# Kernel tuning notes

Measured on AMD Instinct MI355X. Metric: run time of the kernel, lower is better.

The kernel has to match this reference:

```python
import jax, jax.numpy as jnp
import numpy as np

# Mamba2 config fixed by MambaIndexer.__init__: d_state=64, expand=1, headdim=32
D_MODEL = 1024
D_STATE = 64
EXPAND = 1
D_INNER = EXPAND * D_MODEL          # 1024
HEADDIM = 32
NHEADS = D_INNER // HEADDIM         # 32
D_CONV = 4
NGROUPS = 1
IDX_DIM = 64
SEQ = 2048
CONV_DIM = D_INNER + 2 * NGROUPS * D_STATE            # 1152 (x, B, C share the conv)
D_IN_PROJ = 2 * D_INNER + 2 * NGROUPS * D_STATE + NHEADS  # 2208 (z, xBC, dt)


def setup_inputs() -> dict:
    key = jax.random.key(0)
    ks = jax.random.split(key, 10)
    s = 0.02  # init scale for projection weights
    return {
        "x": jax.random.normal(ks[0], (SEQ, D_MODEL), jnp.float32),
        "W_in": jax.random.normal(ks[1], (D_MODEL, D_IN_PROJ), jnp.float32) * s,
        "conv_w": jax.random.normal(ks[2], (CONV_DIM, D_CONV), jnp.float32) * s,
        "conv_b": jnp.zeros((CONV_DIM,), jnp.float32),
        "dt_bias": jax.random.normal(ks[3], (NHEADS,), jnp.float32) * 0.1,
        "A_log": jax.random.uniform(ks[4], (NHEADS,), jnp.float32, 0.0, 1.5),
        "D": jax.random.normal(ks[5], (NHEADS,), jnp.float32),
        "norm_w": jnp.ones((D_INNER,), jnp.float32),
        "W_out": jax.random.normal(ks[6], (D_INNER, D_MODEL), jnp.float32) * s,
        "Wq": jax.random.normal(ks[7], (D_MODEL, IDX_DIM), jnp.float32) * s,
        "Wk": jax.random.normal(ks[8], (D_MODEL, IDX_DIM), jnp.float32) * s,
    }


def _mamba2(x, W_in, conv_w, conv_b, dt_bias, A_log, D, norm_w, W_out):
    L = x.shape[0]
    zxbcdt = x @ W_in                                   # (L, 2208)
    z = zxbcdt[:, :D_INNER]                             # gate
    xBC = zxbcdt[:, D_INNER:D_INNER + CONV_DIM]
    dt = jax.nn.softplus(zxbcdt[:, D_INNER + CONV_DIM:] + dt_bias)  # (L, H)
    # causal depthwise conv1d over seq, kernel 4, then silu
    conv = jax.lax.conv_general_dilated(
        xBC.T[None],                                    # (1, C, L)
        conv_w[:, None, :],                             # (C, 1, K)
        (1,), [(D_CONV - 1, 0)], feature_group_count=CONV_DIM)
    xBC = jax.nn.silu(conv[0].T + conv_b)               # (L, C)
    xs = xBC[:, :D_INNER].reshape(L, NHEADS, HEADDIM)   # (L, H, P)
    B = xBC[:, D_INNER:D_INNER + D_STATE]               # (L, N), ngroups=1
    C = xBC[:, D_INNER + D_STATE:]                      # (L, N)
    A = -jnp.exp(A_log)                                 # (H,)
    dA = jnp.exp(dt * A)                                # (L, H)
    dBx = jnp.einsum('lh,lhp,ln->lhpn', dt, xs, B)      # (L, H, P, N)

    def step(h, inp):
        dA_t, dBx_t, C_t = inp
        h = dA_t[:, None, None] * h + dBx_t             # (H, P, N)
        return h, jnp.einsum('hpn,n->hp', h, C_t)

    h0 = jnp.zeros((NHEADS, HEADDIM, D_STATE), x.dtype)
    _, y = jax.lax.scan(step, h0, (dA, dBx, C))         # y: (L, H, P)
    y = y + D[:, None] * xs                             # skip connection
    y = y.reshape(L, D_INNER) * jax.nn.silu(z)          # gated
    y = y * jax.lax.rsqrt(jnp.mean(y * y, axis=-1, keepdims=True) + 1e-5) * norm_w
    return y @ W_out                                    # (L, d_model)


def reference(x, W_in, conv_w, conv_b, dt_bias, A_log, D, norm_w, W_out, Wq, Wk):
    L = x.shape[0]
    x_mamba = _mamba2(x, W_in, conv_w, conv_b, dt_bias, A_log, D, norm_w, W_out)
    q = x_mamba @ Wq                                    # (L, idx)
    k = x @ Wk                                          # (L, idx)
    scores = jnp.einsum('ti,si->ts', q, k) * (IDX_DIM ** -0.5)
    mask = jnp.tril(jnp.ones((L, L), dtype=bool))
    return jnp.where(mask, scores, -jnp.inf)
```

## Files before the change

kernel.cpp:

```cpp
#include <hip/hip_runtime.h>
#include <hip/hip_bf16.h>
#include <math.h>
#include <float.h>

#define SEQ 2048
#define DMODEL 1024
#define DINNER 1024
#define DSTATE 64
#define HEADDIM 32
#define NHEADS 32
#define DCONV 4
#define CONVDIM 1152
#define DINPROJ 2208
#define DINPROJ_PAD 2304
#define IDXDIM 64

#define CHUNK 64
#define NCHUNKS (SEQ / CHUNK)

#define MASK_VAL (-1e30f)

typedef unsigned short u16;
typedef __bf16 bf16x8 __attribute__((ext_vector_type(8)));
typedef float f32x4 __attribute__((ext_vector_type(4)));
typedef u16 u16x8 __attribute__((ext_vector_type(8)));

__device__ __forceinline__ u16 f2bf(float x) {
    unsigned int u = __float_as_uint(x);
    u += 0x7FFFu + ((u >> 16) & 1u);
    return (u16)(u >> 16);
}
__device__ __forceinline__ float bf2f(u16 u) {
    return __uint_as_float(((unsigned int)u) << 16);
}
__device__ __forceinline__ bf16x8 asbf(u16x8 v) {
    union { u16x8 u; bf16x8 b; } c; c.u = v; return c.b;
}

__device__ __forceinline__ void gload_lds16(const void* g, void* l) {
    __builtin_amdgcn_global_load_lds(
        (const __attribute__((address_space(1))) void*)g,
        (__attribute__((address_space(3))) void*)l, 16, 0, 0);
}

__global__ __launch_bounds__(256)
void convert_all(const float* __restrict__ x, u16* __restrict__ xb,
                 const float* __restrict__ W_in, u16* __restrict__ Wt_in,
                 const float* __restrict__ Wk, u16* __restrict__ Wt_k) {
    __shared__ float tile[32][33];
    int b = blockIdx.x, tid = threadIdx.x;

    if (b < 2048) {
        int i = (b * 256 + tid) * 4;
        float4 v = *(const float4*)(x + i);
        ushort4 o;
        o.x = f2bf(v.x); o.y = f2bf(v.y); o.z = f2bf(v.z); o.w = f2bf(v.w);
        *(ushort4*)(xb + i) = o;
        return;
    }
    const float* W; u16* Wt; int N, bx, by;
    if (b < 4352) { int l = b - 2048; W = W_in; Wt = Wt_in; N = DINPROJ; bx = l % 72; by = l / 72; }
    else          { int l = b - 4352; W = Wk;   Wt = Wt_k;  N = IDXDIM;  bx = l & 1;  by = l >> 1; }
    int k0 = by * 32, n0 = bx * 32;
    int tj = tid & 31, ti = tid >> 5;
#pragma unroll
    for (int s = 0; s < 4; s++) {
        int i = ti + s * 8;
        float v = 0.f;
        if (n0 + tj < N) v = W[(size_t)(k0 + i) * N + n0 + tj];
        tile[i][tj] = v;
    }
    __syncthreads();
#pragma unroll
    for (int s = 0; s < 4; s++) {
        int i = ti + s * 8;
        Wt[(size_t)(n0 + i) * DMODEL + k0 + tj] = f2bf(tile[tj][i]);
    }
}

template<int BM, int BN, int WM, int WN, bool OUT_BF16>
__device__ __forceinline__
void gemm_body(u16* As, u16* Bs,
               const u16* __restrict__ A, const u16* __restrict__ Bt,
               void* __restrict__ Cout, int N, int K, int bx, int by) {
    constexpr int BK = 64;
    constexpr int SLOTS = BK / 8;
    constexpr int MI = WM / 16, NI = WN / 16;
    constexpr int WCOLS = BN / WN;
    constexpr int A_ISS = (BM * BK * 2) / (256 * 16);
    constexpr int B_ISS = (BN * BK * 2) / (256 * 16);

    const int tid = threadIdx.x;
    const int lane = tid & 63;
    const int wid = tid >> 6;
    const int wbase = wid * 64;
    const int wr = wid / WCOLS, wc = wid % WCOLS;
    const int row0 = by * BM, col0 = bx * BN;

    f32x4 acc[MI][NI];
#pragma unroll
    for (int m = 0; m < MI; m++)
#pragma unroll
        for (int n = 0; n < NI; n++) acc[m][n] = (f32x4){0.f, 0.f, 0.f, 0.f};

    const int lrow = lane & 15, lkg = lane >> 4;

    for (int kb = 0; kb < K; kb += BK) {
#pragma unroll
        for (int i = 0; i < A_ISS; i++) {
            int e = (i * 256 + tid) * 8;
            int r = e / BK;
            int sl = (e >> 3) & (SLOTS - 1);
            int c = ((sl ^ (r & (SLOTS - 1))) << 3);
            gload_lds16(A + (size_t)(row0 + r) * K + kb + c,
                        &As[(i * 256 + wbase) * 8]);
        }
#pragma unroll
        for (int i = 0; i < B_ISS; i++) {
            int e = (i * 256 + tid) * 8;
            int r = e / BK;
            int sl = (e >> 3) & (SLOTS - 1);
            int c = ((sl ^ (r & (SLOTS - 1))) << 3);
            gload_lds16(Bt + (size_t)(col0 + r) * K + kb + c,
                        &Bs[(i * 256 + wbase) * 8]);
        }
        __syncthreads();

#pragma unroll
        for (int ks = 0; ks < BK / 32; ks++) {
            bf16x8 af[MI], bff[NI];
#pragma unroll
            for (int m = 0; m < MI; m++) {
                int row = wr * WM + m * 16 + lrow;
                int koff = ks * 32 + lkg * 8;
                af[m] = *(const bf16x8*)&As[row * BK + (koff ^ ((row & (SLOTS - 1)) << 3))];
            }
#pragma unroll
            for (int n = 0; n < NI; n++) {
                int row = wc * WN + n * 16 + lrow;
                int koff = ks * 32 + lkg * 8;
                bff[n] = *(const bf16x8*)&Bs[row * BK + (koff ^ ((row & (SLOTS - 1)) << 3))];
            }
#pragma unroll
            for (int m = 0; m < MI; m++)
#pragma unroll
                for (int n = 0; n < NI; n++)
                    acc[m][n] = __builtin_amdgcn_mfma_f32_16x16x32_bf16(
                        af[m], bff[n], acc[m][n], 0, 0, 0);
        }
        __syncthreads();
    }

    const int crow = (lane >> 4) * 4;
    const int ccol = lane & 15;
#pragma unroll
    for (int m = 0; m < MI; m++) {
#pragma unroll
        for (int n = 0; n < NI; n++) {
            int col = col0 + wc * WN + n * 16 + ccol;
            if (col < N) {
                size_t base = (size_t)(row0 + wr * WM + m * 16 + crow) * N + col;
#pragma unroll
                for (int r = 0; r < 4; r++) {
                    if (OUT_BF16)
                        ((u16*)Cout)[base + (size_t)r * N] = f2bf(acc[m][n][r]);
                    else
                        ((float*)Cout)[base + (size_t)r * N] = acc[m][n][r];
                }
            }
        }
    }
}

__global__ __launch_bounds__(256)
void gemm1_k(const u16* __restrict__ xb, const u16* __restrict__ Wt_in,
             u16* __restrict__ zx_bf, const u16* __restrict__ Wt_k,
             u16* __restrict__ kb,
             const float* __restrict__ Wq, const float* __restrict__ W_out,
             const float* __restrict__ norm_w, u16* __restrict__ Wt_nq) {
    extern __shared__ __align__(16) u16 sm[];
    int b = blockIdx.x, tid = threadIdx.x;
    if (b < 288) {
        gemm_body<128, 128, 64, 64, true>(sm, sm + 128 * 64, xb, Wt_in, zx_bf,
                                          DINPROJ, DMODEL, b % 18, b / 18);
        return;
    }
    if (b < 304) {
        gemm_body<128, 64, 64, 32, true>(sm, sm + 128 * 64, xb, Wt_k, kb,
                                         IDXDIM, DMODEL, 0, b - 288);
        return;
    }
    float* ftile = (float*)sm;
    u16* Bs = sm + 64 * 64 * 2;
    int d0 = (b - 304) * 64;
    int lane = tid & 63, wid = tid >> 6, lrow = lane & 15, lkg = lane >> 4;
    f32x4 acc[4];
#pragma unroll
    for (int ct = 0; ct < 4; ct++) acc[ct] = (f32x4){0.f, 0.f, 0.f, 0.f};

    for (int k0 = 0; k0 < DMODEL; k0 += 64) {
#pragma unroll
        for (int it = 0; it < 4; it++) {
            int e = it * 256 + tid;
            int r = e >> 4, c4 = e & 15;
            *(float4*)&ftile[r * 64 + c4 * 4] =
                *(const float4*)&Wq[(size_t)(k0 + r) * IDXDIM + c4 * 4];
        }
#pragma unroll
        for (int it = 0; it < 2; it++) {
            int e = it * 256 + tid;
            int d = e >> 3, sl = e & 7;
            const float* src = &W_out[(size_t)(d0 + d) * DMODEL + k0 + sl * 8];
            float4 v0 = *(const float4*)src, v1 = *(const float4*)(src + 4);
            u16x8 v;
            v[0] = f2bf(v0.x); v[1] = f2bf(v0.y); v[2] = f2bf(v0.z); v[3] = f2bf(v0.w);
            v[4] = f2bf(v1.x); v[5] = f2bf(v1.y); v[6] = f2bf(v1.z); v[7] = f2bf(v1.w);
            *(u16x8*)&Bs[d * 64 + ((sl ^ (d & 7)) << 3)] = v;
        }
        __syncthreads();
#pragma unroll
        for (int ks = 0; ks < 2; ks++) {
            int j = wid * 16 + lrow;
            int koff = ks * 32 + lkg * 8;
            u16x8 av;
#pragma unroll
            for (int kk = 0; kk < 8; kk++) av[kk] = f2bf(ftile[(koff + kk) * 64 + j]);
            bf16x8 a = asbf(av);
#pragma unroll
            for (int ct = 0; ct < 4; ct++) {
                int d = ct * 16 + lrow;
                bf16x8 bv = *(const bf16x8*)&Bs[d * 64 + (koff ^ ((d & 7) << 3))];
                acc[ct] = __builtin_amdgcn_mfma_f32_16x16x32_bf16(a, bv, acc[ct], 0, 0, 0);
            }
        }
        __syncthreads();
    }
    int ccol = lane & 15;
#pragma unroll
    for (int ct = 0; ct < 4; ct++)
#pragma unroll
        for (int r = 0; r < 4; r++) {
            int j = wid * 16 + lkg * 4 + r;
            int d = d0 + ct * 16 + ccol;
            Wt_nq[(size_t)j * DMODEL + d] = f2bf(acc[ct][r] * norm_w[d]);
        }
}

__global__ void conv_dt_kernel(const u16* __restrict__ zx_bf,
                               const float* __restrict__ conv_w,
                               const float* __restrict__ conv_b,
                               const float* __restrict__ dt_bias,
                               u16* __restrict__ xs_bf,
                               u16* __restrict__ B_bf,
                               u16* __restrict__ C_bf,
                               float* __restrict__ dt_out) {
    int b = blockIdx.x;
    if (b >= 9216) {
        int idx = (b - 9216) * 256 + threadIdx.x;
        int t = idx >> 5, h = idx & 31;
        float v = bf2f(zx_bf[(size_t)t * DINPROJ + (DINNER + CONVDIM) + h]) + dt_bias[h];
        dt_out[idx] = (v > 20.f) ? v : log1pf(expf(v));
        return;
    }
    int idx = b * 256 + threadIdx.x;
    int t = idx / CONVDIM, c = idx % CONVDIM;
    float4 w = *(const float4*)&conv_w[c * 4];
    const u16* src = zx_bf + DINNER + c;
    float acc = conv_b[c];
    float wj[4] = {w.x, w.y, w.z, w.w};
#pragma unroll
    for (int j = 0; j < 4; j++) {
        int tt = t - 3 + j;
        if (tt >= 0) acc += bf2f(src[(size_t)tt * DINPROJ]) * wj[j];
    }
    u16 rb = f2bf(acc / (1.f + expf(-acc)));
    if (c < DINNER) xs_bf[(size_t)t * DINNER + c] = rb;
    else if (c < DINNER + DSTATE) B_bf[(size_t)t * DSTATE + (c - DINNER)] = rb;
    else C_bf[(size_t)t * DSTATE + (c - DINNER - DSTATE)] = rb;
}

__global__ __launch_bounds__(256)
void ssd_state_kernel(const u16* __restrict__ xs_bf,
                      const u16* __restrict__ B_bf,
                      const float* __restrict__ dt,
                      const float* __restrict__ A_log,
                      float* __restrict__ S,
                      float* __restrict__ Pc) {
    int bid = blockIdx.x;
    int c = bid >> 5, h = bid & 31;
    int t0 = c * CHUNK;
    __shared__ __align__(16) u16 Xwt[HEADDIM * CHUNK];
    __shared__ __align__(16) u16 Bt[DSTATE * CHUNK];
    __shared__ float w_lds[CHUNK];
    int tid = threadIdx.x, lane = tid & 63;

    if (tid < 64) {
        float Ah = -__expf(A_log[h]);
        float dv = dt[(t0 + tid) * NHEADS + h];
        float sv = dv * Ah;
#pragma unroll
        for (int d = 1; d < 64; d <<= 1) {
            float o = __shfl_up(sv, d, 64);
            if (lane >= d) sv += o;
        }
        float s63 = __shfl(sv, 63, 64);
        w_lds[tid] = __expf(s63 - sv) * dv;
        if (tid == 63) Pc[c * NHEADS + h] = __expf(sv);
    }
    __syncthreads();

#pragma unroll
    for (int it = 0; it < 8; it++) {
        int e = it * 256 + tid;
        int j = e >> 5, p = e & 31;
        float xv = bf2f(xs_bf[(size_t)(t0 + j) * DINNER + h * HEADDIM + p]) * w_lds[j];
        Xwt[p * 64 + (j ^ ((p & 7) << 3))] = f2bf(xv);
    }
#pragma unroll
    for (int it = 0; it < 16; it++) {
        int e = it * 256 + tid;
        int j = e >> 6, n = e & 63;
        Bt[n * 64 + (j ^ ((n & 7) << 3))] = B_bf[(size_t)(t0 + j) * DSTATE + n];
    }
    __syncthreads();

    int wid = tid >> 6, lrow = lane & 15, lkg = lane >> 4;
    int rt = wid & 1, ctb = (wid >> 1) * 2;
    f32x4 acc[2];
    acc[0] = (f32x4){0.f, 0.f, 0.f, 0.f};
    acc[1] = (f32x4){0.f, 0.f, 0.f, 0.f};
#pragma unroll
    for (int ks = 0; ks < 2; ks++) {
        int p = rt * 16 + lrow;
        bf16x8 av = *(const bf16x8*)&Xwt[p * 64 + ((ks * 32 + lkg * 8) ^ ((p & 7) << 3))];
#pragma unroll
        for (int ci = 0; ci < 2; ci++) {
            int n = (ctb + ci) * 16 + lrow;
            bf16x8 bv = *(const bf16x8*)&Bt[n * 64 + ((ks * 32 + lkg * 8) ^ ((n & 7) << 3))];
            acc[ci] = __builtin_amdgcn_mfma_f32_16x16x32_bf16(av, bv, acc[ci], 0, 0, 0);
        }
    }
    size_t base = (size_t)c * 1024 + h * 32;
#pragma unroll
    for (int ci = 0; ci < 2; ci++)
#pragma unroll
        for (int r = 0; r < 4; r++) {
            int p = rt * 16 + lkg * 4 + r;
            int n = (ctb + ci) * 16 + lrow;
            S[(base + p) * 64 + n] = acc[ci][r];
        }
}

__global__ void state_scan_kernel(float* __restrict__ S,
                                  const float* __restrict__ Pc) {
    int gt = blockIdx.x * blockDim.x + threadIdx.x;
    int w = gt >> 6;
    int lane = gt & 63;
    int h = w >> 5;
    size_t off0 = (size_t)w * 64 + lane;
    float h_run = 0.f;
    float s_next = S[off0];
    float pc_next = Pc[h];
    for (int c = 0; c < NCHUNKS; c++) {
        float s = s_next, pc = pc_next;
        if (c < NCHUNKS - 1) {
            s_next = S[off0 + (size_t)(c + 1) * 65536];
            pc_next = Pc[(c + 1) * NHEADS + h];
        }
        S[off0 + (size_t)c * 65536] = h_run;
        h_run = h_run * pc + s;
    }
}

__global__ __launch_bounds__(256)
void ssd_y_kernel(const u16* __restrict__ xs_bf,
                  const u16* __restrict__ B_bf,
                  const u16* __restrict__ C_bf,
                  const float* __restrict__ dt,
                  const float* __restrict__ A_log,
                  const float* __restrict__ S,
                  const float* __restrict__ Dp,
                  u16* __restrict__ y_bf) {
    int bid = blockIdx.x;
    int c = bid >> 5, h = bid & 31;
    int t0 = c * CHUNK;
    __shared__ __align__(16) u16 Cbf[CHUNK * DSTATE];
    __shared__ __align__(16) u16 Bbf[CHUNK * DSTATE];
    __shared__ __align__(16) u16 Gs[CHUNK * CHUNK];
    __shared__ __align__(16) u16 aCbf[CHUNK * DSTATE];
    __shared__ __align__(16) u16 Xt[HEADDIM * CHUNK];
    __shared__ __align__(16) u16 H0s[HEADDIM * DSTATE];
    __shared__ float s_lds[64], dt_lds[64], a_lds[64];
    int tid = threadIdx.x, lane = tid & 63, wid = tid >> 6;

#pragma unroll
    for (int it = 0; it < 16; it++) {
        int e = it * 256 + tid;
        int i = e >> 6, n = e & 63;
        int nsw = n ^ ((i & 7) << 3);
        Bbf[i * 64 + nsw] = B_bf[(size_t)(t0 + i) * DSTATE + n];
        Cbf[i * 64 + nsw] = C_bf[(size_t)(t0 + i) * DSTATE + n];
    }
#pragma unroll
    for (int it = 0; it < 8; it++) {
        int e = it * 256 + tid;
        int j = e >> 5, p = e & 31;
        Xt[p * 64 + (j ^ ((p & 7) << 3))] =
            xs_bf[(size_t)(t0 + j) * DINNER + h * HEADDIM + p];
    }
#pragma unroll
    for (int it = 0; it < 8; it++) {
        int e = it * 256 + tid;
        int p = e >> 6, n = e & 63;
        H0s[p * 64 + (n ^ ((p & 7) << 3))] =
            f2bf(S[((size_t)c * 1024 + h * 32 + p) * 64 + n]);
    }
    if (tid < 64) {
        float Ah = -__expf(A_log[h]);
        float dv = dt[(t0 + tid) * NHEADS + h];
        float sv = dv * Ah;
#pragma unroll
        for (int d = 1; d < 64; d <<= 1) {
            float o = __shfl_up(sv, d, 64);
            if (lane >= d) sv += o;
        }
        s_lds[tid] = sv;
        dt_lds[tid] = dv;
        a_lds[tid] = __expf(sv);
    }
    __syncthreads();

    int lrow = lane & 15, lkg = lane >> 4;

    f32x4 g[4];
#pragma unroll
    for (int ct = 0; ct < 4; ct++) g[ct] = (f32x4){0.f, 0.f, 0.f, 0.f};
#pragma unroll
    for (int ks = 0; ks < 2; ks++) {
        int i = wid * 16 + lrow;
        bf16x8 af = *(const bf16x8*)&Cbf[i * 64 + ((ks * 32 + lkg * 8) ^ ((i & 7) << 3))];
#pragma unroll
        for (int ct = 0; ct < 4; ct++) {
            int j = ct * 16 + lrow;
            bf16x8 bv = *(const bf16x8*)&Bbf[j * 64 + ((ks * 32 + lkg * 8) ^ ((j & 7) << 3))];
            g[ct] = __builtin_amdgcn_mfma_f32_16x16x32_bf16(af, bv, g[ct], 0, 0, 0);
        }
    }
#pragma unroll
    for (int ct = 0; ct < 4; ct++) {
        int j = ct * 16 + lrow;
        float sj = s_lds[j], dtj = dt_lds[j];
#pragma unroll
        for (int r = 0; r < 4; r++) {
            int i = wid * 16 + lkg * 4 + r;
            float si = s_lds[i];
            float v = (j <= i) ? g[ct][r] * __expf(fminf(si - sj, 0.f)) * dtj : 0.f;
            Gs[i * 64 + (j ^ ((i & 7) << 3))] = f2bf(v);
        }
    }
#pragma unroll
    for (int it = 0; it < 16; it++) {
        int e = it * 256 + tid;
        int i = e >> 6, n = e & 63;
        int idx = i * 64 + (n ^ ((i & 7) << 3));
        aCbf[idx] = f2bf(a_lds[i] * bf2f(Cbf[idx]));
    }
    __syncthreads();

    f32x4 y[2];
    y[0] = (f32x4){0.f, 0.f, 0.f, 0.f};
    y[1] = (f32x4){0.f, 0.f, 0.f, 0.f};
#pragma unroll
    for (int ks = 0; ks < 2; ks++) {
        int i = wid * 16 + lrow;
        int koff = ks * 32 + lkg * 8;
        bf16x8 ga = *(const bf16x8*)&Gs[i * 64 + (koff ^ ((i & 7) << 3))];
        bf16x8 ca = *(const bf16x8*)&aCbf[i * 64 + (koff ^ ((i & 7) << 3))];
#pragma unroll
        for (int ct = 0; ct < 2; ct++) {
            int p = ct * 16 + lrow;
            bf16x8 xv = *(const bf16x8*)&Xt[p * 64 + (koff ^ ((p & 7) << 3))];
            y[ct] = __builtin_amdgcn_mfma_f32_16x16x32_bf16(ga, xv, y[ct], 0, 0, 0);
            bf16x8 hv = *(const bf16x8*)&H0s[p * 64 + (koff ^ ((p & 7) << 3))];
            y[ct] = __builtin_amdgcn_mfma_f32_16x16x32_bf16(ca, hv, y[ct], 0, 0, 0);
        }
    }
    float Dh = Dp[h];
#pragma unroll
    for (int ct = 0; ct < 2; ct++)
#pragma unroll
        for (int r = 0; r < 4; r++) {
            int i = wid * 16 + lkg * 4 + r;
            int p = ct * 16 + lrow;
            float xres = bf2f(Xt[p * 64 + (i ^ ((p & 7) << 3))]);
            y_bf[(size_t)(t0 + i) * DINNER + h * HEADDIM + p] = f2bf(y[ct][r] + Dh * xres);
        }
}

__global__ __launch_bounds__(256)
void rmsq_kernel(const u16* __restrict__ y_bf, const u16* __restrict__ zx_bf,
                 const u16* __restrict__ Wt_nq, u16* __restrict__ qb) {
    __shared__ __align__(16) u16 As[16 * 128];
    __shared__ __align__(16) u16 Bs[64 * 128];
    __shared__ float ssr[16];
    int t0 = blockIdx.x * 16;
    int tid = threadIdx.x, lane = tid & 63, wid = tid >> 6;
    int r = tid >> 4, sl = tid & 15;
    int lrow = lane & 15, lkg = lane >> 4;
    float ss = 0.f;
    f32x4 acc = (f32x4){0.f, 0.f, 0.f, 0.f};

    for (int kc = 0; kc < 8; kc++) {
        int k0 = kc * 128;
#pragma unroll
        for (int it = 0; it < 4; it++) {
            int e = it * 256 + tid;
            int rr = e >> 4, sl2 = e & 15;
            gload_lds16(Wt_nq + (size_t)rr * DMODEL + k0 + ((sl2 ^ (rr & 15)) << 3),
                        &Bs[(it * 256 + wid * 64) * 8]);
        }
        {
            int c0 = sl * 8;
            u16x8 yv = *(const u16x8*)&y_bf[(size_t)(t0 + r) * DINNER + k0 + c0];
            u16x8 zv = *(const u16x8*)&zx_bf[(size_t)(t0 + r) * DINPROJ + k0 + c0];
            u16x8 o;
#pragma unroll
            for (int i = 0; i < 8; i++) {
                float z = bf2f(zv[i]);
                float v = bf2f(yv[i]) * (z / (1.f + __expf(-z)));
                ss += v * v;
                o[i] = f2bf(v);
            }
            *(u16x8*)&As[r * 128 + ((sl ^ r) << 3)] = o;
        }
        __syncthreads();
#pragma unroll
        for (int ks = 0; ks < 4; ks++) {
            int koff = ks * 32 + lkg * 8;
            bf16x8 a = *(const bf16x8*)&As[lrow * 128 + (koff ^ (lrow << 3))];
            int rb = wid * 16 + lrow;
            bf16x8 bv = *(const bf16x8*)&Bs[rb * 128 + (koff ^ ((rb & 15) << 3))];
            acc = __builtin_amdgcn_mfma_f32_16x16x32_bf16(a, bv, acc, 0, 0, 0);
        }
        __syncthreads();
    }
    ss += __shfl_xor(ss, 1, 64);
    ss += __shfl_xor(ss, 2, 64);
    ss += __shfl_xor(ss, 4, 64);
    ss += __shfl_xor(ss, 8, 64);
    if (sl == 0) ssr[r] = ss;
    __syncthreads();
    int ccol = lane & 15;
#pragma unroll
    for (int rr = 0; rr < 4; rr++) {
        int row = lkg * 4 + rr;
        float scale = rsqrtf(ssr[row] / 1024.f + 1e-5f);
        qb[(size_t)(t0 + row) * IDXDIM + wid * 16 + ccol] = f2bf(acc[rr] * scale);
    }
}

__global__ __launch_bounds__(256)
void scores_kernel(const u16* __restrict__ q, const u16* __restrict__ k,
                   float* __restrict__ out) {
    int bx = blockIdx.x, by = blockIdx.y;
    int row0 = by * 64, col0 = bx * 64;
    int tid = threadIdx.x;
    if (bx > by) {
        float4 mv = make_float4(MASK_VAL, MASK_VAL, MASK_VAL, MASK_VAL);
#pragma unroll
        for (int it = 0; it < 4; it++) {
            int e = it * 256 + tid;
            int r = e >> 4, c4 = e & 15;
            *(float4*)&out[(size_t)(row0 + r) * SEQ + col0 + c4 * 4] = mv;
        }
        return;
    }
    __shared__ __align__(16) u16 qs[64 * 64];
    __shared__ __align__(16) u16 kss[64 * 64];
    int lane = tid & 63, wid = tid >> 6, lrow = lane & 15, lkg = lane >> 4;
#pragma unroll
    for (int it = 0; it < 2; it++) {
        int e = (it * 256 + tid) * 8;
        int r = e >> 6, c0 = e & 63;
        int csw = c0 ^ ((r & 7) << 3);
        *(u16x8*)&qs[r * 64 + csw] = *(const u16x8*)&q[(size_t)(row0 + r) * IDXDIM + c0];
        *(u16x8*)&kss[r * 64 + csw] = *(const u16x8*)&k[(size_t)(col0 + r) * IDXDIM + c0];
    }
    __syncthreads();
    f32x4 g[4];
#pragma unroll
    for (int ct = 0; ct < 4; ct++) g[ct] = (f32x4){0.f, 0.f, 0.f, 0.f};
#pragma unroll
    for (int ks = 0; ks < 2; ks++) {
        int i = wid * 16 + lrow;
        int koff = ks * 32 + lkg * 8;
        bf16x8 af = *(const bf16x8*)&qs[i * 64 + (koff ^ ((i & 7) << 3))];
#pragma unroll
        for (int ct = 0; ct < 4; ct++) {
            int j = ct * 16 + lrow;
            bf16x8 bv = *(const bf16x8*)&kss[j * 64 + (koff ^ ((j & 7) << 3))];
            g[ct] = __builtin_amdgcn_mfma_f32_16x16x32_bf16(af, bv, g[ct], 0, 0, 0);
        }
    }
#pragma unroll
    for (int ct = 0; ct < 4; ct++)
#pragma unroll
        for (int r = 0; r < 4; r++) {
            int trow = row0 + wid * 16 + lkg * 4 + r;
            int tcol = col0 + ct * 16 + lrow;
            out[(size_t)trow * SEQ + tcol] =
                (tcol <= trow) ? g[ct][r] * 0.125f : MASK_VAL;
        }
}

extern "C" void kernel_launch(void* const* d_in, const int* in_sizes, int n_in,
                              void* d_out, int out_size, void* d_ws, size_t ws_size,
                              hipStream_t stream) {
    const float* x       = (const float*)d_in[0];
    const float* W_in    = (const float*)d_in[1];
    const float* conv_w  = (const float*)d_in[2];
    const float* conv_b  = (const float*)d_in[3];
    const float* dt_bias = (const float*)d_in[4];
    const float* A_log   = (const float*)d_in[5];
    const float* Dp      = (const float*)d_in[6];
    const float* norm_w  = (const float*)d_in[7];
    const float* W_out   = (const float*)d_in[8];
    const float* Wq      = (const float*)d_in[9];
    const float* Wk      = (const float*)d_in[10];
    float* out = (float*)d_out;
    float* ws = (float*)d_ws;

    float* S  = ws;
    float* Pc = S + (size_t)SEQ * DINNER;
    float* dt = Pc + 1024;
    u16* ub = (u16*)(dt + SEQ * NHEADS);
    u16* zx_bf = ub;                 ub += (size_t)SEQ * DINPROJ;
    u16* y_bf  = ub;                 ub += (size_t)SEQ * DINNER;
    u16* xs_bf = ub;                 ub += (size_t)SEQ * DINNER;
    u16* B_bf  = ub;                 ub += SEQ * DSTATE;
    u16* C_bf  = ub;                 ub += SEQ * DSTATE;
    u16* qb    = ub;                 ub += SEQ * IDXDIM;
    u16* kb    = ub;                 ub += SEQ * IDXDIM;
    u16* xb    = ub;                 ub += (size_t)SEQ * DMODEL;
    u16* Wt_in = ub;                 ub += (size_t)DINPROJ_PAD * DMODEL;
    u16* Wt_k  = ub;                 ub += IDXDIM * DMODEL;
    u16* Wt_nq = ub;                 ub += IDXDIM * DMODEL;

    convert_all<<<4416, 256, 0, stream>>>(x, xb, W_in, Wt_in, Wk, Wt_k);

    gemm1_k<<<320, 256, 32768, stream>>>(xb, Wt_in, zx_bf, Wt_k, kb,
                                         Wq, W_out, norm_w, Wt_nq);

    conv_dt_kernel<<<9472, 256, 0, stream>>>(zx_bf, conv_w, conv_b, dt_bias,
                                             xs_bf, B_bf, C_bf, dt);

    ssd_state_kernel<<<NCHUNKS * NHEADS, 256, 0, stream>>>(xs_bf, B_bf, dt, A_log, S, Pc);
    state_scan_kernel<<<256, 256, 0, stream>>>(S, Pc);
    ssd_y_kernel<<<NCHUNKS * NHEADS, 256, 0, stream>>>(
        xs_bf, B_bf, C_bf, dt, A_log, S, Dp, y_bf);

    rmsq_kernel<<<SEQ / 16, 256, 0, stream>>>(y_bf, zx_bf, Wt_nq, qb);

    scores_kernel<<<dim3(SEQ / 64, SEQ / 64), 256, 0, stream>>>(qb, kb, out);
}
```

Before: 82.52 us.

## Store chunk states in bf16, retile in-proj GEMM, move mask fill earlier

Chunk states S are now stored as bf16 instead of fp32, which halves the traffic through ssd_state, state_scan and ssd_y. The scan still accumulates in fp32 but rounds each prefix state to bf16 on store. The in-projection GEMM switches from 128x128 to 128x64 tiles, doubling the block count to 608 for better CU occupancy and using less LDS. Writing the upper-triangle mask tiles moves into the early convert kernel, so the scores kernel only launches real work for lower-triangle tiles.

```diff
diff --git a/kernel.cpp b/kernel.cpp
--- a/kernel.cpp
+++ b/kernel.cpp
@@ -46,7 +46,8 @@
 __global__ __launch_bounds__(256)
 void convert_all(const float* __restrict__ x, u16* __restrict__ xb,
                  const float* __restrict__ W_in, u16* __restrict__ Wt_in,
-                 const float* __restrict__ Wk, u16* __restrict__ Wt_k) {
+                 const float* __restrict__ Wk, u16* __restrict__ Wt_k,
+                 float* __restrict__ out) {
     __shared__ float tile[32][33];
     int b = blockIdx.x, tid = threadIdx.x;
 
@@ -58,23 +59,40 @@
         *(ushort4*)(xb + i) = o;
         return;
     }
-    const float* W; u16* Wt; int N, bx, by;
-    if (b < 4352) { int l = b - 2048; W = W_in; Wt = Wt_in; N = DINPROJ; bx = l % 72; by = l / 72; }
-    else          { int l = b - 4352; W = Wk;   Wt = Wt_k;  N = IDXDIM;  bx = l & 1;  by = l >> 1; }
-    int k0 = by * 32, n0 = bx * 32;
-    int tj = tid & 31, ti = tid >> 5;
-#pragma unroll
-    for (int s = 0; s < 4; s++) {
-        int i = ti + s * 8;
-        float v = 0.f;
-        if (n0 + tj < N) v = W[(size_t)(k0 + i) * N + n0 + tj];
-        tile[i][tj] = v;
-    }
-    __syncthreads();
-#pragma unroll
-    for (int s = 0; s < 4; s++) {
-        int i = ti + s * 8;
-        Wt[(size_t)(n0 + i) * DMODEL + k0 + tj] = f2bf(tile[tj][i]);
+    if (b < 4416) {
+        const float* W; u16* Wt; int N, bx, by;
+        if (b < 4352) { int l = b - 2048; W = W_in; Wt = Wt_in; N = DINPROJ; bx = l % 72; by = l / 72; }
+        else          { int l = b - 4352; W = Wk;   Wt = Wt_k;  N = IDXDIM;  bx = l & 1;  by = l >> 1; }
+        int k0 = by * 32, n0 = bx * 32;
+        int tj = tid & 31, ti = tid >> 5;
+#pragma unroll
+        for (int s = 0; s < 4; s++) {
+            int i = ti + s * 8;
+            float v = 0.f;
+            if (n0 + tj < N) v = W[(size_t)(k0 + i) * N + n0 + tj];
+            tile[i][tj] = v;
+        }
+        __syncthreads();
+#pragma unroll
+        for (int s = 0; s < 4; s++) {
+            int i = ti + s * 8;
+            Wt[(size_t)(n0 + i) * DMODEL + k0 + tj] = f2bf(tile[tj][i]);
+        }
+        return;
+    }
+    {
+        int id = b - 4416;
+        int by = 0, rem = id;
+        while (rem >= 31 - by) { rem -= 31 - by; by++; }
+        int bx = by + 1 + rem;
+        int row0 = by * 64, col0 = bx * 64;
+        float4 mv = make_float4(MASK_VAL, MASK_VAL, MASK_VAL, MASK_VAL);
+#pragma unroll
+        for (int it = 0; it < 4; it++) {
+            int e = it * 256 + tid;
+            int r = e >> 4, c4 = e & 15;
+            *(float4*)&out[(size_t)(row0 + r) * SEQ + col0 + c4 * 4] = mv;
+        }
     }
 }
 
@@ -180,19 +198,19 @@
              const float* __restrict__ norm_w, u16* __restrict__ Wt_nq) {
     extern __shared__ __align__(16) u16 sm[];
     int b = blockIdx.x, tid = threadIdx.x;
-    if (b < 288) {
-        gemm_body<128, 128, 64, 64, true>(sm, sm + 128 * 64, xb, Wt_in, zx_bf,
-                                          DINPROJ, DMODEL, b % 18, b / 18);
+    if (b < 576) {
+        gemm_body<128, 64, 64, 32, true>(sm, sm + 128 * 64, xb, Wt_in, zx_bf,
+                                         DINPROJ, DMODEL, b % 36, b / 36);
         return;
     }
-    if (b < 304) {
+    if (b < 592) {
         gemm_body<128, 64, 64, 32, true>(sm, sm + 128 * 64, xb, Wt_k, kb,
-                                         IDXDIM, DMODEL, 0, b - 288);
+                                         IDXDIM, DMODEL, 0, b - 576);
         return;
     }
     float* ftile = (float*)sm;
     u16* Bs = sm + 64 * 64 * 2;
-    int d0 = (b - 304) * 64;
+    int d0 = (b - 592) * 64;
     int lane = tid & 63, wid = tid >> 6, lrow = lane & 15, lkg = lane >> 4;
     f32x4 acc[4];
 #pragma unroll
@@ -284,7 +302,7 @@
                       const u16* __restrict__ B_bf,
                       const float* __restrict__ dt,
                       const float* __restrict__ A_log,
-                      float* __restrict__ S,
+                      u16* __restrict__ S_bf,
                       float* __restrict__ Pc) {
     int bid = blockIdx.x;
     int c = bid >> 5, h = bid & 31;
@@ -347,11 +365,11 @@
         for (int r = 0; r < 4; r++) {
             int p = rt * 16 + lkg * 4 + r;
             int n = (ctb + ci) * 16 + lrow;
-            S[(base + p) * 64 + n] = acc[ci][r];
-        }
-}
-
-__global__ void state_scan_kernel(float* __restrict__ S,
+            S_bf[(base + p) * 64 + n] = f2bf(acc[ci][r]);
+        }
+}
+
+__global__ void state_scan_kernel(u16* __restrict__ S_bf,
                                   const float* __restrict__ Pc) {
     int gt = blockIdx.x * blockDim.x + threadIdx.x;
     int w = gt >> 6;
@@ -359,15 +377,15 @@
     int h = w >> 5;
     size_t off0 = (size_t)w * 64 + lane;
     float h_run = 0.f;
-    float s_next = S[off0];
+    float s_next = bf2f(S_bf[off0]);
     float pc_next = Pc[h];
     for (int c = 0; c < NCHUNKS; c++) {
         float s = s_next, pc = pc_next;
         if (c < NCHUNKS - 1) {
-            s_next = S[off0 + (size_t)(c + 1) * 65536];
+            s_next = bf2f(S_bf[off0 + (size_t)(c + 1) * 65536]);
             pc_next = Pc[(c + 1) * NHEADS + h];
         }
-        S[off0 + (size_t)c * 65536] = h_run;
+        S_bf[off0 + (size_t)c * 65536] = f2bf(h_run);
         h_run = h_run * pc + s;
     }
 }
@@ -378,7 +396,7 @@
                   const u16* __restrict__ C_bf,
                   const float* __restrict__ dt,
                   const float* __restrict__ A_log,
-                  const float* __restrict__ S,
+                  const u16* __restrict__ S_bf,
                   const float* __restrict__ Dp,
                   u16* __restrict__ y_bf) {
     int bid = blockIdx.x;
@@ -413,7 +431,7 @@
         int e = it * 256 + tid;
         int p = e >> 6, n = e & 63;
         H0s[p * 64 + (n ^ ((p & 7) << 3))] =
-            f2bf(S[((size_t)c * 1024 + h * 32 + p) * 64 + n]);
+            S_bf[((size_t)c * 1024 + h * 32 + p) * 64 + n];
     }
     if (tid < 64) {
         float Ah = -__expf(A_log[h]);
@@ -563,18 +581,9 @@
 void scores_kernel(const u16* __restrict__ q, const u16* __restrict__ k,
                    float* __restrict__ out) {
     int bx = blockIdx.x, by = blockIdx.y;
+    if (bx > by) return;
     int row0 = by * 64, col0 = bx * 64;
     int tid = threadIdx.x;
-    if (bx > by) {
-        float4 mv = make_float4(MASK_VAL, MASK_VAL, MASK_VAL, MASK_VAL);
-#pragma unroll
-        for (int it = 0; it < 4; it++) {
-            int e = it * 256 + tid;
-            int r = e >> 4, c4 = e & 15;
-            *(float4*)&out[(size_t)(row0 + r) * SEQ + col0 + c4 * 4] = mv;
-        }
-        return;
-    }
     __shared__ __align__(16) u16 qs[64 * 64];
     __shared__ __align__(16) u16 kss[64 * 64];
     int lane = tid & 63, wid = tid >> 6, lrow = lane & 15, lkg = lane >> 4;
@@ -630,10 +639,10 @@
     float* out = (float*)d_out;
     float* ws = (float*)d_ws;
 
-    float* S  = ws;
-    float* Pc = S + (size_t)SEQ * DINNER;
+    float* Pc = ws;
     float* dt = Pc + 1024;
     u16* ub = (u16*)(dt + SEQ * NHEADS);
+    u16* S_bf  = ub;                 ub += (size_t)SEQ * DINNER;
     u16* zx_bf = ub;                 ub += (size_t)SEQ * DINPROJ;
     u16* y_bf  = ub;                 ub += (size_t)SEQ * DINNER;
     u16* xs_bf = ub;                 ub += (size_t)SEQ * DINNER;
@@ -646,18 +655,18 @@
     u16* Wt_k  = ub;                 ub += IDXDIM * DMODEL;
     u16* Wt_nq = ub;                 ub += IDXDIM * DMODEL;
 
-    convert_all<<<4416, 256, 0, stream>>>(x, xb, W_in, Wt_in, Wk, Wt_k);
-
-    gemm1_k<<<320, 256, 32768, stream>>>(xb, Wt_in, zx_bf, Wt_k, kb,
+    convert_all<<<4912, 256, 0, stream>>>(x, xb, W_in, Wt_in, Wk, Wt_k, out);
+
+    gemm1_k<<<608, 256, 24576, stream>>>(xb, Wt_in, zx_bf, Wt_k, kb,
                                          Wq, W_out, norm_w, Wt_nq);
 
     conv_dt_kernel<<<9472, 256, 0, stream>>>(zx_bf, conv_w, conv_b, dt_bias,
                                              xs_bf, B_bf, C_bf, dt);
 
-    ssd_state_kernel<<<NCHUNKS * NHEADS, 256, 0, stream>>>(xs_bf, B_bf, dt, A_log, S, Pc);
-    state_scan_kernel<<<256, 256, 0, stream>>>(S, Pc);
+    ssd_state_kernel<<<NCHUNKS * NHEADS, 256, 0, stream>>>(xs_bf, B_bf, dt, A_log, S_bf, Pc);
+    state_scan_kernel<<<256, 256, 0, stream>>>(S_bf, Pc);
     ssd_y_kernel<<<NCHUNKS * NHEADS, 256, 0, stream>>>(
-        xs_bf, B_bf, C_bf, dt, A_log, S, Dp, y_bf);
+        xs_bf, B_bf, C_bf, dt, A_log, S_bf, Dp, y_bf);
 
     rmsq_kernel<<<SEQ / 16, 256, 0, stream>>>(y_bf, zx_bf, Wt_nq, qb);
 
```

Result: no change. 82.52 us (-0.0%).
